# Optimization experiments

Hardware: AMD Instinct MI355X
Metric: run time of the kernel (lower is better)

## Reference

```python
import jax, jax.numpy as jnp
import numpy as np

EPS = 1e-5


def _conv1x1(h, w, b):
    # 1x1 conv == per-pixel matmul: (b,c,h,w) x (o,c) -> (b,o,h,w)
    return jnp.einsum('bchw,oc->bohw', h, w) + b[None, :, None, None]


def setup_inputs() -> dict:
    key = jax.random.key(0)
    ks = jax.random.split(key, 7)
    B, C, H, W = 4, 512, 64, 64
    s = 0.02
    return {
        'x': jax.random.normal(ks[0], (B, C, H, W), dtype=jnp.float32),
        'wq': jax.random.normal(ks[1], (C, C), dtype=jnp.float32) * s,
        'bq': jax.random.normal(ks[2], (C,), dtype=jnp.float32) * s,
        'wk': jax.random.normal(ks[3], (C, C), dtype=jnp.float32) * s,
        'bk': jax.random.normal(ks[4], (C,), dtype=jnp.float32) * s,
        'wv': jax.random.normal(ks[5], (C, C), dtype=jnp.float32) * s,
        'bv': jax.random.normal(ks[6], (C,), dtype=jnp.float32) * s,
    }


def reference(x, wq, bq, wk, bk, wv, bv):
    B, C, H, W = x.shape
    # InstanceNorm2d (affine=False): normalize over spatial dims per (b, c)
    mu = jnp.mean(x, axis=(2, 3), keepdims=True)
    var = jnp.var(x, axis=(2, 3), keepdims=True)  # biased, matches torch
    h_ = (x - mu) * jax.lax.rsqrt(var + EPS)

    q = _conv1x1(h_, wq, bq).reshape(B, C, H * W)  # (b, c, n)
    k = _conv1x1(h_, wk, bk).reshape(B, C, H * W)
    v = _conv1x1(h_, wv, bv).reshape(B, C, H * W)

    scale = float(int(C)) ** (-0.5)
    attn = jnp.einsum('bcq,bck->bqk', q, k) * scale  # (b, n_q, n_k)
    attn = jax.nn.softmax(attn, axis=-1)
    # torch: bmm(v, attn.permute(0,2,1)) -> A[b,c,q] = sum_k v[b,c,k] * attn[b,q,k]
    A = jnp.einsum('bck,bqk->bcq', v, attn).reshape(B, C, H, W)
    return x + A
```

## Files before the change

kernel.cpp:

```cpp
#include <hip/hip_runtime.h>
#include <hip/hip_bf16.h>
#include <cstdint>

#define B_ 4
#define C_ 512
#define N_ 4096

typedef unsigned short u16;
typedef __bf16 bf16x8 __attribute__((ext_vector_type(8)));
typedef float f32x4 __attribute__((ext_vector_type(4)));

union U16B { uint4 u; bf16x8 v; };

__device__ __forceinline__ bf16x8 ld16g(const u16* p) {
  U16B t; t.u = *(const uint4*)p; return t.v;
}

__device__ __forceinline__ u16 f2bf(float f) {
  uint32_t u = __builtin_bit_cast(uint32_t, f);
  u = (u + 0x7FFFu + ((u >> 16) & 1u)) >> 16;
  return (u16)u;
}
__device__ __forceinline__ float bf2f(u16 h) {
  uint32_t u = ((uint32_t)h) << 16;
  return __builtin_bit_cast(float, u);
}

typedef const __attribute__((address_space(1))) uint32_t* gas_p;
typedef __attribute__((address_space(3))) uint32_t* las_p;
__device__ __forceinline__ void gld16(const void* g, void* l) {
  __builtin_amdgcn_global_load_lds((gas_p)g, (las_p)l, 16, 0, 0);
}

#define SCEXP 0.06376149809794171f

__global__ __launch_bounds__(256) void cvt_w(const float* __restrict__ w, u16* __restrict__ o) {
  int i = blockIdx.x * 256 + threadIdx.x;
  float4 v = ((const float4*)w)[i];
  ushort4 r;
  r.x = f2bf(v.x); r.y = f2bf(v.y); r.z = f2bf(v.z); r.w = f2bf(v.w);
  ((ushort4*)o)[i] = r;
}

__global__ __launch_bounds__(1024) void pack_bias(const float* __restrict__ bq,
    const float* __restrict__ bk, float* __restrict__ o) {
  int i = threadIdx.x;
  o[i] = (i < 512) ? bq[i] : bk[i - 512];
}

__global__ __launch_bounds__(256) void inorm_stats(const float* __restrict__ x,
    float* __restrict__ mu, float* __restrict__ rstd) {
  int bc = blockIdx.x;
  const float4* p = (const float4*)(x + (size_t)bc * N_);
  float s = 0.f, ss = 0.f;
  for (int i = threadIdx.x; i < N_ / 4; i += 256) {
    float4 v = p[i];
    s  += v.x + v.y + v.z + v.w;
    ss += v.x * v.x + v.y * v.y + v.z * v.z + v.w * v.w;
  }
#pragma unroll
  for (int off = 32; off > 0; off >>= 1) {
    s  += __shfl_down(s, off);
    ss += __shfl_down(ss, off);
  }
  __shared__ float as_[4], ass_[4];
  if ((threadIdx.x & 63) == 0) { as_[threadIdx.x >> 6] = s; ass_[threadIdx.x >> 6] = ss; }
  __syncthreads();
  if (threadIdx.x == 0) {
    float S  = as_[0] + as_[1] + as_[2] + as_[3];
    float SS = ass_[0] + ass_[1] + ass_[2] + ass_[3];
    float m  = S * (1.f / N_);
    float var = SS * (1.f / N_) - m * m;
    mu[bc] = m;
    rstd[bc] = rsqrtf(var + 1e-5f);
  }
}

__global__ __launch_bounds__(256) void norm_transpose(const float* __restrict__ x,
    const float* __restrict__ mu, const float* __restrict__ rstd, u16* __restrict__ hT) {
  __shared__ u16 tile[64][66];
  int b = blockIdx.z, c0 = blockIdx.y * 64, n0 = blockIdx.x * 64;
  int tn = threadIdx.x & 63, t4 = threadIdx.x >> 6;
  const float* xb = x + ((size_t)b * C_ + c0) * N_ + n0;
#pragma unroll
  for (int it = 0; it < 16; ++it) {
    int c = t4 + it * 4;
    float m  = mu[b * C_ + c0 + c];
    float rs = rstd[b * C_ + c0 + c];
    tile[c][tn] = f2bf((xb[(size_t)c * N_ + tn] - m) * rs);
  }
  __syncthreads();
  u16* hTb = hT + ((size_t)b * N_ + n0) * C_ + c0;
#pragma unroll
  for (int it = 0; it < 16; ++it) {
    int n = t4 + it * 4;
    hTb[(size_t)n * C_ + tn] = tile[tn][n];
  }
}

#define EPI_BCOL 0
#define EPI_BROW 1

template<int EPI>
__global__ __launch_bounds__(256) void gemm128(
    const u16* __restrict__ A, const u16* __restrict__ B,
    const float* __restrict__ aux, void* __restrict__ Out,
    int klen, int lda, int ldb, int ldo,
    long sAz, long sBz, long sOz)
{
  int z = blockIdx.z;
  const u16* Ab = A + (size_t)z * sAz;
  const u16* Bb = B + (size_t)z * sBz;
  int m0 = blockIdx.x * 128, n0 = blockIdx.y * 128;
  int t = threadIdx.x, w = t >> 6, l = t & 63;
  int wr = w >> 1, wc = w & 1;
  int l16 = l & 15, lg = l >> 4;

  __shared__ char smem[65536];

  int srow = t >> 3;
  int scol = ((t & 7) << 4) ^ ((srow & 7) << 4);
  size_t ldaB = (size_t)lda * 2, ldbB = (size_t)ldb * 2;

  f32x4 acc[4][4] = {};
  int nsteps = klen >> 6;

#define STAGE(step, d) {                                                     \
    size_t kbyte = (size_t)(step) * 128 + scol;                              \
    char* lb = smem + (d) * 32768;                                           \
    _Pragma("unroll")                                                        \
    for (int i = 0; i < 4; ++i) {                                            \
      int row = i * 32 + srow;                                               \
      gld16((const char*)Ab + (size_t)(m0 + row) * ldaB + kbyte,             \
            lb + (size_t)(i * 256 + t) * 16);                                \
      gld16((const char*)Bb + (size_t)(n0 + row) * ldbB + kbyte,             \
            lb + 16384 + (size_t)(i * 256 + t) * 16);                        \
    }                                                                        \
  }

  STAGE(0, 0);
  __syncthreads();
  int cur = 0;
  int sw = (l16 & 7) << 4;
  for (int s = 0; s < nsteps; ++s) {
    if (s + 1 < nsteps) STAGE(s + 1, cur ^ 1);
    const char* Al = smem + cur * 32768;
    const char* Bl = Al + 16384;
#pragma unroll
    for (int kc = 0; kc < 2; ++kc) {
      int cb = (kc * 64 + lg * 16) ^ sw;
      bf16x8 af[4], bf[4];
#pragma unroll
      for (int mf = 0; mf < 4; ++mf)
        af[mf] = *(const bf16x8*)(Al + (wr * 64 + mf * 16 + l16) * 128 + cb);
#pragma unroll
      for (int nf = 0; nf < 4; ++nf)
        bf[nf] = *(const bf16x8*)(Bl + (wc * 64 + nf * 16 + l16) * 128 + cb);
#pragma unroll
      for (int mf = 0; mf < 4; ++mf)
#pragma unroll
        for (int nf = 0; nf < 4; ++nf)
          acc[mf][nf] = __builtin_amdgcn_mfma_f32_16x16x32_bf16(af[mf], bf[nf], acc[mf][nf], 0, 0, 0);
    }
    __syncthreads();
    cur ^= 1;
  }
#undef STAGE

  u16* ob = (u16*)Out + (size_t)z * sOz;
  float bc[4];
  if constexpr (EPI == EPI_BCOL) {
#pragma unroll
    for (int nf = 0; nf < 4; ++nf) bc[nf] = aux[n0 + wc * 64 + nf * 16 + l16];
  }
#pragma unroll
  for (int mf = 0; mf < 4; ++mf) {
#pragma unroll
    for (int nf = 0; nf < 4; ++nf) {
      int col = n0 + wc * 64 + nf * 16 + l16;
#pragma unroll
      for (int r = 0; r < 4; ++r) {
        int row = m0 + wr * 64 + mf * 16 + lg * 4 + r;
        float v = acc[mf][nf][r] + (EPI == EPI_BCOL ? bc[nf] : aux[row]);
        ob[(size_t)row * ldo + col] = f2bf(v);
      }
    }
  }
}

__global__ __launch_bounds__(256, 4) void exp128(
    const u16* __restrict__ qk, float* __restrict__ dsumAll, u16* __restrict__ Pall)
{
  int fid = blockIdx.x;
  int rid = (fid & 7) * 512 + (fid >> 3);
  int z = rid >> 10;
  int r10 = rid & 1023;
  int st = r10 >> 6, w6 = r10 & 63;
  int m0 = ((st >> 2) * 8 + (w6 >> 3)) * 128;
  int n0 = ((st & 3) * 8 + (w6 & 7)) * 128;

  const u16* Ab = qk + (size_t)z * ((size_t)N_ * 1024);
  const u16* Bb = Ab + 512;
  float* dsum = dsumAll + (size_t)z * N_;
  u16* Pp = Pall + (size_t)z * (size_t)N_ * N_;

  int t = threadIdx.x, w = t >> 6, l = t & 63;
  int wr = w >> 1, wc = w & 1;
  int l16 = l & 15, lg = l >> 4;

  __shared__ char smem[32768];

  f32x4 acc[4][4] = {};

#define STG(step, d) {                                                       \
    size_t kb = (size_t)(step) * 64;                                         \
    char* lb = smem + (d) * 16384;                                           \
    _Pragma("unroll")                                                        \
    for (int i = 0; i < 2; ++i) {                                            \
      int s2 = i * 256 + t;                                                  \
      int row = s2 >> 2;                                                     \
      int sc = (((s2 & 3) - row) & 3) << 4;                                  \
      gld16((const char*)Ab + (size_t)(m0 + row) * 2048 + kb + sc,           \
            lb + (size_t)s2 * 16);                                           \
      gld16((const char*)Bb + (size_t)(n0 + row) * 2048 + kb + sc,           \
            lb + 8192 + (size_t)s2 * 16);                                    \
    }                                                                        \
  }

  STG(0, 0);
  int cur = 0;
  int rg = ((lg + l16) & 3) << 4;
#pragma unroll
  for (int s = 0; s < 16; ++s) {
    if (s < 15) {
      STG(s + 1, cur ^ 1);
      asm volatile("s_waitcnt vmcnt(4)" ::: "memory");
    } else {
      asm volatile("s_waitcnt vmcnt(0)" ::: "memory");
    }
    __builtin_amdgcn_s_barrier();
    __builtin_amdgcn_sched_barrier(0);
    const char* Al = smem + cur * 16384;
    const char* Bl = Al + 8192;
    bf16x8 af[4], bf[4];
#pragma unroll
    for (int mf = 0; mf < 4; ++mf)
      af[mf] = *(const bf16x8*)(Al + (wr * 64 + mf * 16 + l16) * 64 + rg);
#pragma unroll
    for (int nf = 0; nf < 4; ++nf)
      bf[nf] = *(const bf16x8*)(Bl + (wc * 64 + nf * 16 + l16) * 64 + rg);
#pragma unroll
    for (int mf = 0; mf < 4; ++mf)
#pragma unroll
      for (int nf = 0; nf < 4; ++nf)
        acc[mf][nf] = __builtin_amdgcn_mfma_f32_16x16x32_bf16(af[mf], bf[nf], acc[mf][nf], 0, 0, 0);
    __builtin_amdgcn_sched_barrier(0);
    __builtin_amdgcn_s_barrier();
    cur ^= 1;
  }
#undef STG

#pragma unroll
  for (int mf = 0; mf < 4; ++mf) {
#pragma unroll
    for (int r = 0; r < 4; ++r) {
      int row = wr * 64 + mf * 16 + lg * 4 + r;
      int swz = ((row >> 2) & 3) << 5;
      float rs = 0.f;
#pragma unroll
      for (int nf = 0; nf < 4; ++nf) {
        int colb = wc * 128 + nf * 32 + l16 * 2;
        float p = __builtin_amdgcn_exp2f(acc[mf][nf][r] * SCEXP);
        u16 pb = f2bf(p);
        *(u16*)(smem + row * 256 + (colb ^ swz)) = pb;
        rs += bf2f(pb);
      }
      rs += __shfl_xor(rs, 1); rs += __shfl_xor(rs, 2);
      rs += __shfl_xor(rs, 4); rs += __shfl_xor(rs, 8);
      if (l16 == 0) atomicAdd(&dsum[m0 + row], rs);
    }
  }
  __syncthreads();
#pragma unroll
  for (int it = 0; it < 8; ++it) {
    int idx = it * 256 + t;
    int row = idx >> 4, g = idx & 15;
    uint4 v = *(const uint4*)(smem + row * 256 + ((g * 16) ^ (((row >> 2) & 3) << 5)));
    *(uint4*)(Pp + ((size_t)(m0 + row) * N_ + n0 + g * 8)) = v;
  }
}

__global__ __launch_bounds__(256, 4) void pv128(
    const u16* __restrict__ vM, const u16* __restrict__ P,
    const float* __restrict__ denom, const float* __restrict__ x,
    float* __restrict__ out)
{
  int fid = blockIdx.x;
  int rid = (fid & 7) * 64 + (fid >> 3);
  int z = rid >> 7;
  int r7 = rid & 127;
  int n0 = (r7 >> 2) * 128;
  int m0 = (r7 & 3) * 128;

  const u16* Ab = vM + (size_t)z * ((size_t)C_ * N_);
  const u16* Bb = P + (size_t)z * ((size_t)N_ * N_);
  const float* db = denom + (size_t)z * N_;
  const float* xb = x + (size_t)z * ((size_t)C_ * N_);
  float* ob = out + (size_t)z * ((size_t)C_ * N_);

  int t = threadIdx.x, w = t >> 6, l = t & 63;
  int wr = w >> 1, wc = w & 1;
  int l16 = l & 15, lg = l >> 4;

  __shared__ char smem[32768];

  f32x4 acc[4][4] = {};

#define STG(step, d) {                                                       \
    size_t kb = (size_t)(step) * 64;                                         \
    char* lb = smem + (d) * 16384;                                           \
    _Pragma("unroll")                                                        \
    for (int i = 0; i < 2; ++i) {                                            \
      int s2 = i * 256 + t;                                                  \
      int row = s2 >> 2;                                                     \
      int sc = (((s2 & 3) - row) & 3) << 4;                                  \
      gld16((const char*)Ab + (size_t)(m0 + row) * 8192 + kb + sc,           \
            lb + (size_t)s2 * 16);                                           \
      gld16((const char*)Bb + (size_t)(n0 + row) * 8192 + kb + sc,           \
            lb + 8192 + (size_t)s2 * 16);                                    \
    }                                                                        \
  }

  STG(0, 0);
  int cur = 0;
  int rg = ((lg + l16) & 3) << 4;
#pragma unroll 2
  for (int s = 0; s < 128; ++s) {
    if (s < 127) {
      STG(s + 1, cur ^ 1);
      asm volatile("s_waitcnt vmcnt(4)" ::: "memory");
    } else {
      asm volatile("s_waitcnt vmcnt(0)" ::: "memory");
    }
    __builtin_amdgcn_s_barrier();
    __builtin_amdgcn_sched_barrier(0);
    const char* Al = smem + cur * 16384;
    const char* Bl = Al + 8192;
    bf16x8 af[4], bf[4];
#pragma unroll
    for (int mf = 0; mf < 4; ++mf)
      af[mf] = *(const bf16x8*)(Al + (wr * 64 + mf * 16 + l16) * 64 + rg);
#pragma unroll
    for (int nf = 0; nf < 4; ++nf)
      bf[nf] = *(const bf16x8*)(Bl + (wc * 64 + nf * 16 + l16) * 64 + rg);
#pragma unroll
    for (int mf = 0; mf < 4; ++mf)
#pragma unroll
      for (int nf = 0; nf < 4; ++nf)
        acc[mf][nf] = __builtin_amdgcn_mfma_f32_16x16x32_bf16(af[mf], bf[nf], acc[mf][nf], 0, 0, 0);
    __builtin_amdgcn_sched_barrier(0);
    __builtin_amdgcn_s_barrier();
    cur ^= 1;
  }
#undef STG

  float rd[4];
#pragma unroll
  for (int nf = 0; nf < 4; ++nf)
    rd[nf] = 1.0f / db[n0 + wc * 64 + nf * 16 + l16];
#pragma unroll
  for (int mf = 0; mf < 4; ++mf) {
#pragma unroll
    for (int r = 0; r < 4; ++r) {
      int row = m0 + wr * 64 + mf * 16 + lg * 4 + r;
#pragma unroll
      for (int nf = 0; nf < 4; ++nf) {
        int col = n0 + wc * 64 + nf * 16 + l16;
        size_t o = (size_t)row * N_ + col;
        ob[o] = xb[o] + acc[mf][nf][r] * rd[nf];
      }
    }
  }
}

__global__ __launch_bounds__(256) void gemm_abT(
    const u16* __restrict__ A, const u16* __restrict__ Bm,
    const float* __restrict__ bias, u16* __restrict__ out,
    int ldo, int bias_is_row)
{
  int w = threadIdx.x >> 6, l = threadIdx.x & 63;
  int l16 = l & 15, lg = l >> 4;
  int m0 = blockIdx.x * 128 + (w >> 1) * 64;
  int n0 = blockIdx.y * 128 + (w & 1) * 64;
  f32x4 acc[4][4] = {};
  const u16* Ab = A  + (size_t)(m0 + l16) * 512 + lg * 8;
  const u16* Bb = Bm + (size_t)(n0 + l16) * 512 + lg * 8;
  for (int kc = 0; kc < 512; kc += 32) {
    bf16x8 af[4], bf[4];
#pragma unroll
    for (int i = 0; i < 4; ++i) af[i] = ld16g(Ab + (size_t)(i * 16) * 512 + kc);
#pragma unroll
    for (int j = 0; j < 4; ++j) bf[j] = ld16g(Bb + (size_t)(j * 16) * 512 + kc);
#pragma unroll
    for (int i = 0; i < 4; ++i)
#pragma unroll
      for (int j = 0; j < 4; ++j)
        acc[i][j] = __builtin_amdgcn_mfma_f32_16x16x32_bf16(af[i], bf[j], acc[i][j], 0, 0, 0);
  }
#pragma unroll
  for (int i = 0; i < 4; ++i) {
#pragma unroll
    for (int j = 0; j < 4; ++j) {
      int col = n0 + j * 16 + l16;
#pragma unroll
      for (int r = 0; r < 4; ++r) {
        int row = m0 + i * 16 + lg * 4 + r;
        float v = acc[i][j][r] + (bias_is_row ? bias[row] : bias[col]);
        out[(size_t)row * ldo + col] = f2bf(v);
      }
    }
  }
}

#define NQ 32
#define NKB 64
__global__ __launch_bounds__(512) void attn_kernel(
    const u16* __restrict__ qT, const u16* __restrict__ kT, const u16* __restrict__ vM,
    const float* __restrict__ x, float* __restrict__ out)
{
  int b = blockIdx.y;
  int nq0 = blockIdx.x * NQ;
  const u16* qTb = qT + (size_t)b * N_ * C_;
  const u16* kTb = kT + (size_t)b * N_ * C_;
  const u16* vb  = vM + (size_t)b * C_ * N_;
  const float* xb = x + (size_t)b * C_ * N_;
  float* ob = out + (size_t)b * C_ * N_;

  int tid = threadIdx.x;
  int w = tid >> 6, l = tid & 63, l16 = l & 15, lg = l >> 4;
  int nqf = w & 1, nkf = w >> 1;
  int c0 = w * 64;

  __shared__ u16 qlds[32][520];
  __shared__ u16 Plds[32][72];
  __shared__ float dpart[32][16];
  __shared__ float dfin[32];

  for (int idx = tid; idx < 32 * 64; idx += 512) {
    int row = idx >> 6, cg = idx & 63;
    *(uint4*)&qlds[row][cg * 8] = *(const uint4*)(qTb + (size_t)(nq0 + row) * C_ + cg * 8);
  }
  __syncthreads();

  f32x4 acc[2][4] = {};
  float dreg = 0.f;
  int drow = tid >> 4, dcol = (tid & 15) * 4;

  for (int nk0 = 0; nk0 < N_; nk0 += NKB) {
    f32x4 s = {0.f, 0.f, 0.f, 0.f};
    const u16* krow = kTb + (size_t)(nk0 + nkf * 16 + l16) * C_ + lg * 8;
#pragma unroll 4
    for (int kc = 0; kc < 16; ++kc) {
      U16B tq; tq.u = *(const uint4*)&qlds[nqf * 16 + l16][kc * 32 + lg * 8];
      bf16x8 kf = ld16g(krow + kc * 32);
      s = __builtin_amdgcn_mfma_f32_16x16x32_bf16(tq.v, kf, s, 0, 0, 0);
    }
    __syncthreads();
#pragma unroll
    for (int r = 0; r < 4; ++r) {
      float p = __builtin_amdgcn_exp2f(s[r] * SCEXP);
      Plds[nqf * 16 + lg * 4 + r][nkf * 16 + l16] = f2bf(p);
    }
    __syncthreads();
#pragma unroll
    for (int r = 0; r < 4; ++r) dreg += bf2f(Plds[drow][dcol + r]);
#pragma unroll
    for (int kk = 0; kk < 2; ++kk) {
      bf16x8 pf[2];
#pragma unroll
      for (int i = 0; i < 2; ++i) {
        U16B t2; t2.u = *(const uint4*)&Plds[i * 16 + l16][kk * 32 + lg * 8];
        pf[i] = t2.v;
      }
#pragma unroll
      for (int j = 0; j < 4; ++j) {
        bf16x8 vf = ld16g(vb + (size_t)(c0 + j * 16 + l16) * N_ + nk0 + kk * 32 + lg * 8);
#pragma unroll
        for (int i = 0; i < 2; ++i)
          acc[i][j] = __builtin_amdgcn_mfma_f32_16x16x32_bf16(pf[i], vf, acc[i][j], 0, 0, 0);
      }
    }
  }

  dpart[drow][tid & 15] = dreg;
  __syncthreads();
  if (tid < 32) {
    float s2 = 0.f;
#pragma unroll
    for (int g = 0; g < 16; ++g) s2 += dpart[tid][g];
    dfin[tid] = s2;
  }
  __syncthreads();

#pragma unroll
  for (int i = 0; i < 2; ++i) {
    float dinv[4];
#pragma unroll
    for (int r = 0; r < 4; ++r) dinv[r] = 1.f / dfin[i * 16 + lg * 4 + r];
    int nbase = nq0 + i * 16 + lg * 4;
#pragma unroll
    for (int j = 0; j < 4; ++j) {
      int c = c0 + j * 16 + l16;
      float4 xv = *(const float4*)(xb + (size_t)c * N_ + nbase);
      float4 o;
      o.x = xv.x + acc[i][j][0] * dinv[0];
      o.y = xv.y + acc[i][j][1] * dinv[1];
      o.z = xv.z + acc[i][j][2] * dinv[2];
      o.w = xv.w + acc[i][j][3] * dinv[3];
      *(float4*)(ob + (size_t)c * N_ + nbase) = o;
    }
  }
}

extern "C" void kernel_launch(void* const* d_in, const int* in_sizes, int n_in,
                              void* d_out, int out_size, void* d_ws, size_t ws_size,
                              hipStream_t stream) {
  (void)in_sizes; (void)n_in; (void)out_size;
  const float* x  = (const float*)d_in[0];
  const float* wq = (const float*)d_in[1];
  const float* bq = (const float*)d_in[2];
  const float* wk = (const float*)d_in[3];
  const float* bk = (const float*)d_in[4];
  const float* wv = (const float*)d_in[5];
  const float* bv = (const float*)d_in[6];
  float* out = (float*)d_out;
  char* ws = (char*)d_ws;

  const size_t NC = (size_t)N_ * C_;
  const size_t NEED = 203489280;

  if (ws_size >= NEED) {
    u16*   wbf_q = (u16*)(ws);
    u16*   wbf_k = (u16*)(ws + 524288);
    u16*   wbf_v = (u16*)(ws + 1048576);
    float* bqk   = (float*)(ws + 1572864);
    float* mu    = (float*)(ws + 1581056);
    float* rstd  = (float*)(ws + 1589248);
    u16*   hT    = (u16*)(ws + 1597440);
    u16*   qkT   = (u16*)(ws + 18874368);
    u16*   vM    = (u16*)(ws + 52428800);
    float* denom = (float*)(ws + 69206016);
    u16*   P     = (u16*)(ws + 69271552);

    cvt_w<<<256, 256, 0, stream>>>(wq, wbf_q);
    cvt_w<<<256, 256, 0, stream>>>(wk, wbf_k);
    cvt_w<<<256, 256, 0, stream>>>(wv, wbf_v);
    pack_bias<<<1, 1024, 0, stream>>>(bq, bk, bqk);
    inorm_stats<<<B_ * C_, 256, 0, stream>>>(x, mu, rstd);
    norm_transpose<<<dim3(N_ / 64, C_ / 64, B_), 256, 0, stream>>>(x, mu, rstd, hT);
    hipMemsetAsync(denom, 0, 4 * N_ * sizeof(float), stream);

    gemm128<EPI_BCOL><<<dim3(32, 8, 4), 256, 0, stream>>>(
        hT, wbf_q, bqk, qkT, 512, 512, 512, 1024, (long)NC, 0, (long)N_ * 1024);
    gemm128<EPI_BROW><<<dim3(4, 32, 4), 256, 0, stream>>>(
        wbf_v, hT, bv, vM, 512, 512, 512, 4096, 0, (long)NC, (long)NC);

    exp128<<<4096, 256, 0, stream>>>(qkT, denom, P);

    pv128<<<512, 256, 0, stream>>>(vM, P, denom, x, out);
  } else {
    u16*   wbf_q = (u16*)(ws);
    u16*   wbf_k = (u16*)(ws + 524288);
    u16*   wbf_v = (u16*)(ws + 1048576);
    float* mu    = (float*)(ws + 1572864);
    float* rstd  = (float*)(ws + 1581056);
    u16*   hT    = (u16*)(ws + 1589248);
    u16*   qT    = (u16*)(ws + 18366464);
    u16*   kT    = (u16*)(ws + 35143680);
    u16*   vM    = (u16*)(ws + 51920896);

    cvt_w<<<256, 256, 0, stream>>>(wq, wbf_q);
    cvt_w<<<256, 256, 0, stream>>>(wk, wbf_k);
    cvt_w<<<256, 256, 0, stream>>>(wv, wbf_v);
    inorm_stats<<<B_ * C_, 256, 0, stream>>>(x, mu, rstd);
    norm_transpose<<<dim3(N_ / 64, C_ / 64, B_), 256, 0, stream>>>(x, mu, rstd, hT);

    for (int b = 0; b < B_; ++b) {
      const u16* hTb = hT + (size_t)b * NC;
      u16* qTb = qT + (size_t)b * NC;
      u16* kTb = kT + (size_t)b * NC;
      u16* vMb = vM + (size_t)b * NC;
      gemm_abT<<<dim3(N_ / 128, C_ / 128), 256, 0, stream>>>(hTb, wbf_q, bq, qTb, C_, 0);
      gemm_abT<<<dim3(N_ / 128, C_ / 128), 256, 0, stream>>>(hTb, wbf_k, bk, kTb, C_, 0);
      gemm_abT<<<dim3(C_ / 128, N_ / 128), 256, 0, stream>>>(wbf_v, hTb, bv, vMb, N_, 1);
    }
    attn_kernel<<<dim3(N_ / NQ, B_), 512, 0, stream>>>(qT, kT, vM, x, out);
  }
}
```

Baseline: 241.5 us.

## Triple-buffer LDS tiles in exp and PV GEMMs with a single barrier per step

Both the QK^T/exp kernel and the PV kernel move from a double-buffered to a triple-buffered LDS pipeline. Loads run two K-steps ahead, and the trailing barrier in each iteration is removed, leaving one barrier per step. The LDS swizzle changes from an add-based rotation to an XOR pattern. The extra buffer raises LDS to 48KB per block, and the launch bounds drop from 4 to 3 blocks per CU, trading occupancy for deeper latency hiding and less synchronisation.

```diff
diff --git a/kernel.cpp b/kernel.cpp
--- a/kernel.cpp
+++ b/kernel.cpp
@@ -188,7 +188,39 @@
   }
 }
 
-__global__ __launch_bounds__(256, 4) void exp128(
+
+#define STG32(Ab, Bb, ldab, step, lb) {                                      \
+    size_t kb = (size_t)(step) * 64;                                         \
+    _Pragma("unroll")                                                        \
+    for (int i = 0; i < 2; ++i) {                                            \
+      int s2 = i * 256 + t;                                                  \
+      int row = s2 >> 2;                                                     \
+      int sc = (((s2 & 3) ^ ((row >> 1) & 3)) & 3) << 4;                     \
+      gld16((const char*)(Ab) + (size_t)(m0 + row) * (ldab) + kb + sc,       \
+            (lb) + (size_t)s2 * 16);                                         \
+      gld16((const char*)(Bb) + (size_t)(n0 + row) * (ldab) + kb + sc,       \
+            (lb) + 8192 + (size_t)s2 * 16);                                  \
+    }                                                                        \
+  }
+
+#define COMP32(lb) {                                                         \
+    const char* Al = (lb);                                                   \
+    const char* Bl = (lb) + 8192;                                            \
+    bf16x8 af[4], bf[4];                                                     \
+    _Pragma("unroll")                                                        \
+    for (int mf = 0; mf < 4; ++mf)                                           \
+      af[mf] = *(const bf16x8*)(Al + (wr * 64 + mf * 16 + l16) * 64 + rg);   \
+    _Pragma("unroll")                                                        \
+    for (int nf = 0; nf < 4; ++nf)                                           \
+      bf[nf] = *(const bf16x8*)(Bl + (wc * 64 + nf * 16 + l16) * 64 + rg);   \
+    _Pragma("unroll")                                                        \
+    for (int mf = 0; mf < 4; ++mf)                                           \
+      _Pragma("unroll")                                                      \
+      for (int nf = 0; nf < 4; ++nf)                                         \
+        acc[mf][nf] = __builtin_amdgcn_mfma_f32_16x16x32_bf16(af[mf], bf[nf], acc[mf][nf], 0, 0, 0); \
+  }
+
+__global__ __launch_bounds__(256, 3) void exp128(
     const u16* __restrict__ qk, float* __restrict__ dsumAll, u16* __restrict__ Pall)
 {
   int fid = blockIdx.x;
@@ -208,58 +240,32 @@
   int wr = w >> 1, wc = w & 1;
   int l16 = l & 15, lg = l >> 4;
 
-  __shared__ char smem[32768];
+  __shared__ char smem[49152];
 
   f32x4 acc[4][4] = {};
-
-#define STG(step, d) {                                                       \
-    size_t kb = (size_t)(step) * 64;                                         \
-    char* lb = smem + (d) * 16384;                                           \
-    _Pragma("unroll")                                                        \
-    for (int i = 0; i < 2; ++i) {                                            \
-      int s2 = i * 256 + t;                                                  \
-      int row = s2 >> 2;                                                     \
-      int sc = (((s2 & 3) - row) & 3) << 4;                                  \
-      gld16((const char*)Ab + (size_t)(m0 + row) * 2048 + kb + sc,           \
-            lb + (size_t)s2 * 16);                                           \
-      gld16((const char*)Bb + (size_t)(n0 + row) * 2048 + kb + sc,           \
-            lb + 8192 + (size_t)s2 * 16);                                    \
-    }                                                                        \
-  }
-
-  STG(0, 0);
-  int cur = 0;
-  int rg = ((lg + l16) & 3) << 4;
-#pragma unroll
-  for (int s = 0; s < 16; ++s) {
-    if (s < 15) {
-      STG(s + 1, cur ^ 1);
-      asm volatile("s_waitcnt vmcnt(4)" ::: "memory");
-    } else {
-      asm volatile("s_waitcnt vmcnt(0)" ::: "memory");
-    }
+  int rg = ((lg ^ ((l16 >> 1) & 3)) & 3) << 4;
+
+  char* buf0 = smem;
+  char* buf1 = smem + 16384;
+  char* buf2 = smem + 32768;
+
+  STG32(Ab, Bb, 2048, 0, buf0);
+  STG32(Ab, Bb, 2048, 1, buf1);
+#pragma unroll
+  for (int s = 0; s < 15; ++s) {
+    asm volatile("s_waitcnt vmcnt(4)" ::: "memory");
     __builtin_amdgcn_s_barrier();
     __builtin_amdgcn_sched_barrier(0);
-    const char* Al = smem + cur * 16384;
-    const char* Bl = Al + 8192;
-    bf16x8 af[4], bf[4];
-#pragma unroll
-    for (int mf = 0; mf < 4; ++mf)
-      af[mf] = *(const bf16x8*)(Al + (wr * 64 + mf * 16 + l16) * 64 + rg);
-#pragma unroll
-    for (int nf = 0; nf < 4; ++nf)
-      bf[nf] = *(const bf16x8*)(Bl + (wc * 64 + nf * 16 + l16) * 64 + rg);
-#pragma unroll
-    for (int mf = 0; mf < 4; ++mf)
-#pragma unroll
-      for (int nf = 0; nf < 4; ++nf)
-        acc[mf][nf] = __builtin_amdgcn_mfma_f32_16x16x32_bf16(af[mf], bf[nf], acc[mf][nf], 0, 0, 0);
-    __builtin_amdgcn_sched_barrier(0);
-    __builtin_amdgcn_s_barrier();
-    cur ^= 1;
-  }
-#undef STG
-
+    if (s + 2 < 16) STG32(Ab, Bb, 2048, s + 2, buf2);
+    COMP32(buf0);
+    char* tmp = buf0; buf0 = buf1; buf1 = buf2; buf2 = tmp;
+  }
+  asm volatile("s_waitcnt vmcnt(0)" ::: "memory");
+  __builtin_amdgcn_s_barrier();
+  __builtin_amdgcn_sched_barrier(0);
+  COMP32(buf0);
+
+  __syncthreads();
 #pragma unroll
   for (int mf = 0; mf < 4; ++mf) {
 #pragma unroll
@@ -290,7 +296,7 @@
   }
 }
 
-__global__ __launch_bounds__(256, 4) void pv128(
+__global__ __launch_bounds__(256, 3) void pv128(
     const u16* __restrict__ vM, const u16* __restrict__ P,
     const float* __restrict__ denom, const float* __restrict__ x,
     float* __restrict__ out)
@@ -312,57 +318,30 @@
   int wr = w >> 1, wc = w & 1;
   int l16 = l & 15, lg = l >> 4;
 
-  __shared__ char smem[32768];
+  __shared__ char smem[49152];
 
   f32x4 acc[4][4] = {};
-
-#define STG(step, d) {                                                       \
-    size_t kb = (size_t)(step) * 64;                                         \
-    char* lb = smem + (d) * 16384;                                           \
-    _Pragma("unroll")                                                        \
-    for (int i = 0; i < 2; ++i) {                                            \
-      int s2 = i * 256 + t;                                                  \
-      int row = s2 >> 2;                                                     \
-      int sc = (((s2 & 3) - row) & 3) << 4;                                  \
-      gld16((const char*)Ab + (size_t)(m0 + row) * 8192 + kb + sc,           \
-            lb + (size_t)s2 * 16);                                           \
-      gld16((const char*)Bb + (size_t)(n0 + row) * 8192 + kb + sc,           \
-            lb + 8192 + (size_t)s2 * 16);                                    \
-    }                                                                        \
-  }
-
-  STG(0, 0);
-  int cur = 0;
-  int rg = ((lg + l16) & 3) << 4;
-#pragma unroll 2
-  for (int s = 0; s < 128; ++s) {
-    if (s < 127) {
-      STG(s + 1, cur ^ 1);
-      asm volatile("s_waitcnt vmcnt(4)" ::: "memory");
-    } else {
-      asm volatile("s_waitcnt vmcnt(0)" ::: "memory");
-    }
+  int rg = ((lg ^ ((l16 >> 1) & 3)) & 3) << 4;
+
+  char* buf0 = smem;
+  char* buf1 = smem + 16384;
+  char* buf2 = smem + 32768;
+
+  STG32(Ab, Bb, 8192, 0, buf0);
+  STG32(Ab, Bb, 8192, 1, buf1);
+#pragma unroll 3
+  for (int s = 0; s < 127; ++s) {
+    asm volatile("s_waitcnt vmcnt(4)" ::: "memory");
     __builtin_amdgcn_s_barrier();
     __builtin_amdgcn_sched_barrier(0);
-    const char* Al = smem + cur * 16384;
-    const char* Bl = Al + 8192;
-    bf16x8 af[4], bf[4];
-#pragma unroll
-    for (int mf = 0; mf < 4; ++mf)
-      af[mf] = *(const bf16x8*)(Al + (wr * 64 + mf * 16 + l16) * 64 + rg);
-#pragma unroll
-    for (int nf = 0; nf < 4; ++nf)
-      bf[nf] = *(const bf16x8*)(Bl + (wc * 64 + nf * 16 + l16) * 64 + rg);
-#pragma unroll
-    for (int mf = 0; mf < 4; ++mf)
-#pragma unroll
-      for (int nf = 0; nf < 4; ++nf)
-        acc[mf][nf] = __builtin_amdgcn_mfma_f32_16x16x32_bf16(af[mf], bf[nf], acc[mf][nf], 0, 0, 0);
-    __builtin_amdgcn_sched_barrier(0);
-    __builtin_amdgcn_s_barrier();
-    cur ^= 1;
-  }
-#undef STG
+    if (s + 2 < 128) STG32(Ab, Bb, 8192, s + 2, buf2);
+    COMP32(buf0);
+    char* tmp = buf0; buf0 = buf1; buf1 = buf2; buf2 = tmp;
+  }
+  asm volatile("s_waitcnt vmcnt(0)" ::: "memory");
+  __builtin_amdgcn_s_barrier();
+  __builtin_amdgcn_sched_barrier(0);
+  COMP32(buf0);
 
   float rd[4];
 #pragma unroll
```

After: 240.8 us. About the same (-0.3%).
